# Kernel tuning notes

Measured on AMD Instinct MI355X. Metric: run time of the kernel, lower is better.

## Reference

```python
import jax, jax.numpy as jnp
import numpy as np

N_BCH = 64      # walkers / batch
N_DIM = 64      # total columns in col_var
N_COL = 32      # masked collective variables
N_HIL = 50000   # stored Gaussian hills (history)
WDT = 0.3
HGT0 = 0.02
GAM0 = 10.0
PBC_LEN = 2.0 * np.pi


def gaussian_inner(pbc, prc, cen, hgt, col):
    # col: (B, C); cen, prc: (H, B, C); hgt: (H, B); pbc: (C,)
    diff = col[None, :, :] - cen                      # (H, B, C)
    # minimum-image PBC wrap (only for periodic columns, pbc > 0)
    diff = jnp.where(pbc > 0, diff - pbc * jnp.round(diff / pbc), diff)
    dist2 = jnp.sum(prc * diff * diff, axis=-1)       # (H, B)
    return jnp.sum(hgt * jnp.exp(-0.5 * dist2), axis=0)  # (B,)


def setup_inputs() -> dict:
    key = jax.random.key(0)
    k = jax.random.split(key, 6)
    col_var = jax.random.normal(k[0], (N_BCH, N_DIM), dtype=jnp.float32)
    # hill centers live on the periodic domain
    mtd_cen = jax.random.uniform(k[1], (N_HIL, N_BCH, N_COL), jnp.float32,
                                 -PBC_LEN / 2, PBC_LEN / 2)
    prc_val = 1.0 / (WDT * WDT)
    mtd_prc = jnp.full((N_HIL, N_BCH, N_COL), prc_val, dtype=jnp.float32)
    # well-tempered heights decay over history; random positive heights
    mtd_hgt = HGT0 * jax.random.uniform(k[2], (N_HIL, N_BCH), jnp.float32, 0.1, 1.0)
    kbt = jax.random.uniform(k[3], (N_BCH,), jnp.float32, 0.5, 1.0)
    # module buffers (from __init__ kwargs)
    prc = jnp.full((N_COL,), prc_val, dtype=jnp.float32)   # 1/(wdt*wdt)
    hgt = jnp.asarray(HGT0, dtype=jnp.float32)
    gam = jnp.asarray(GAM0, dtype=jnp.float32)
    pbc = jnp.full((N_COL,), PBC_LEN, dtype=jnp.float32)
    msk = jnp.arange(N_COL, dtype=jnp.int32)
    return {"col_var": col_var, "mtd_cen": mtd_cen, "mtd_prc": mtd_prc,
            "mtd_hgt": mtd_hgt, "kbt": kbt, "prc": prc, "hgt": hgt,
            "gam": gam, "pbc": pbc, "msk": msk}


def reference(col_var, mtd_cen, mtd_prc, mtd_hgt, kbt, prc, hgt, gam, pbc, msk):
    col = col_var[:, msk]                              # (B, C)
    eng = gaussian_inner(pbc, mtd_prc, mtd_cen, mtd_hgt, col)  # (B,)
    # new_gaussian_wtmtd: exponential (well-tempered) height rescale
    det = gam * kbt - kbt                              # (B,)
    hgt_wt = hgt * jnp.exp(-eng / det)                 # (B,)
    prc_new = jnp.broadcast_to(prc[None, :], col.shape)  # (B, C)
    return col, prc_new, hgt_wt
```

## Files before the change

### kernel.cpp

```cpp
#include <hip/hip_runtime.h>

#define N_BCH 64
#define N_DIM 64
#define N_COL 32

typedef float f32x4 __attribute__((ext_vector_type(4)));

__global__ __launch_bounds__(512, 8) void wtmd_main(
    const float* __restrict__ col_var,
    const float* __restrict__ mtd_cen,
    const float* __restrict__ mtd_prc,
    const float* __restrict__ mtd_hgt,
    const float* __restrict__ pbc,
    const int*   __restrict__ msk,
    float*       __restrict__ partial,
    int n_hil)
{
    const int t  = threadIdx.x;
    const int b  = t >> 3;
    const int c0 = (4 * t) & 31;

    float col[4], pb[4], ipb[4];
#pragma unroll
    for (int j = 0; j < 4; ++j) {
        const int c = c0 + j;
        col[j] = col_var[b * N_DIM + msk[c]];
        const float p = pbc[c];
        pb[j]  = p;
        ipb[j] = (p > 0.f) ? (1.0f / p) : 0.f;
    }

    float acc = 0.f;
    const int stride = gridDim.x;

    for (int h = blockIdx.x; h < n_hil; h += stride) {
        const size_t base = (size_t)h * (N_BCH * N_COL) + 4 * (size_t)t;
        const f32x4 cen = __builtin_nontemporal_load((const f32x4*)(mtd_cen + base));
        const f32x4 pr  = __builtin_nontemporal_load((const f32x4*)(mtd_prc + base));
        const float hg  = __builtin_nontemporal_load(mtd_hgt + (size_t)h * N_BCH + b);

        float s = 0.f;
#pragma unroll
        for (int j = 0; j < 4; ++j) {
            float d = col[j] - cen[j];
            d -= pb[j] * rintf(d * ipb[j]);
            s = fmaf(pr[j] * d, d, s);
        }

#pragma unroll
        for (int m = 1; m < 8; m <<= 1)
            s += __shfl_xor(s, m);

        acc += hg * __expf(-0.5f * s);
    }

    if ((t & 7) == 0)
        partial[(size_t)b * stride + blockIdx.x] = acc;
}

__global__ __launch_bounds__(256) void wtmd_epi(
    const float* __restrict__ col_var,
    const float* __restrict__ kbt,
    const float* __restrict__ prc,
    const float* __restrict__ hgt,
    const float* __restrict__ gam,
    const int*   __restrict__ msk,
    const float* __restrict__ partial,
    int nblocks,
    float*       __restrict__ out)
{
    __shared__ float red[256];
    const int t = threadIdx.x;
    const int b = t & 63;
    const int s = t >> 6;

    const float* row = partial + (size_t)b * nblocks;
    float acc = 0.f;
    for (int g = 4 * s; g < nblocks; g += 16) {
        const f32x4 v = *(const f32x4*)(row + g);
        acc += (v[0] + v[1]) + (v[2] + v[3]);
    }
    red[t] = acc;
    __syncthreads();

    if (t < 64) {
        const float eng = (red[t] + red[t + 64]) + (red[t + 128] + red[t + 192]);
        const float k   = kbt[t];
        const float det = gam[0] * k - k;
        out[4096 + t] = hgt[0] * __expf(-eng / det);
    }

    for (int i = t; i < N_BCH * N_COL; i += 256) {
        const int bb = i >> 5;
        const int c  = i & 31;
        out[i]        = col_var[bb * N_DIM + msk[c]];
        out[2048 + i] = prc[c];
    }
}

extern "C" void kernel_launch(void* const* d_in, const int* in_sizes, int n_in,
                              void* d_out, int out_size, void* d_ws, size_t ws_size,
                              hipStream_t stream) {
    const float* col_var = (const float*)d_in[0];
    const float* mtd_cen = (const float*)d_in[1];
    const float* mtd_prc = (const float*)d_in[2];
    const float* mtd_hgt = (const float*)d_in[3];
    const float* kbt     = (const float*)d_in[4];
    const float* prc     = (const float*)d_in[5];
    const float* hgt     = (const float*)d_in[6];
    const float* gam     = (const float*)d_in[7];
    const float* pbc     = (const float*)d_in[8];
    const int*   msk     = (const int*)d_in[9];
    float* out     = (float*)d_out;
    float* partial = (float*)d_ws;

    const int n_hil = in_sizes[3] / N_BCH;

    int nblocks = 1024;
    const size_t per_block = (size_t)N_BCH * sizeof(float);
    if (ws_size < (size_t)nblocks * per_block)
        nblocks = (int)(ws_size / per_block);
    nblocks &= ~3;
    if (nblocks < 4) nblocks = 4;

    wtmd_main<<<nblocks, 512, 0, stream>>>(col_var, mtd_cen, mtd_prc, mtd_hgt,
                                           pbc, msk, partial, n_hil);
    wtmd_epi<<<1, 256, 0, stream>>>(col_var, kbt, prc, hgt, gam, msk,
                                    partial, nblocks, out);
}
```

Measured before the change: 149.8 us.

## Fuse epilogue into main kernel via last-block atomic counter and unroll hill loop by two

Folds the separate reduction/epilogue kernel into the main kernel: each block writes its partials, bumps an atomic counter, and the last block to finish does the final reduction and the exp rescale. The masked column and precision copies move to block 0. The hill loop is also unrolled by two so each thread has two independent load sets in flight. This adds a memset launch for the counter, threadfences and an atomic per block in exchange for dropping the second kernel launch.

```diff
diff --git a/kernel.cpp b/kernel.cpp
--- a/kernel.cpp
+++ b/kernel.cpp
@@ -6,19 +6,35 @@
 
 typedef float f32x4 __attribute__((ext_vector_type(4)));
 
-__global__ __launch_bounds__(512, 8) void wtmd_main(
+__global__ __launch_bounds__(512, 8) void wtmd_fused(
     const float* __restrict__ col_var,
     const float* __restrict__ mtd_cen,
     const float* __restrict__ mtd_prc,
     const float* __restrict__ mtd_hgt,
+    const float* __restrict__ kbt,
+    const float* __restrict__ prc,
+    const float* __restrict__ hgt,
+    const float* __restrict__ gam,
     const float* __restrict__ pbc,
     const int*   __restrict__ msk,
     float*       __restrict__ partial,
-    int n_hil)
+    unsigned*    __restrict__ counter,
+    int n_hil,
+    float*       __restrict__ out)
 {
     const int t  = threadIdx.x;
     const int b  = t >> 3;
     const int c0 = (4 * t) & 31;
+    const int stride = gridDim.x;
+
+    if (blockIdx.x == 0) {
+        for (int i = t; i < N_BCH * N_COL; i += 512) {
+            const int bb = i >> 5;
+            const int c  = i & 31;
+            out[i]        = col_var[bb * N_DIM + msk[c]];
+            out[2048 + i] = prc[c];
+        }
+    }
 
     float col[4], pb[4], ipb[4];
 #pragma unroll
@@ -31,70 +47,85 @@
     }
 
     float acc = 0.f;
-    const int stride = gridDim.x;
+    const int off4t = 4 * t;
 
-    for (int h = blockIdx.x; h < n_hil; h += stride) {
-        const size_t base = (size_t)h * (N_BCH * N_COL) + 4 * (size_t)t;
-        const f32x4 cen = __builtin_nontemporal_load((const f32x4*)(mtd_cen + base));
-        const f32x4 pr  = __builtin_nontemporal_load((const f32x4*)(mtd_prc + base));
-        const float hg  = __builtin_nontemporal_load(mtd_hgt + (size_t)h * N_BCH + b);
+    int h = blockIdx.x;
+    for (; h + stride < n_hil; h += 2 * stride) {
+        const size_t base0 = (size_t)h * (N_BCH * N_COL) + off4t;
+        const size_t base1 = (size_t)(h + stride) * (N_BCH * N_COL) + off4t;
+        const f32x4 cen0 = __builtin_nontemporal_load((const f32x4*)(mtd_cen + base0));
+        const f32x4 pr0  = __builtin_nontemporal_load((const f32x4*)(mtd_prc + base0));
+        const f32x4 cen1 = __builtin_nontemporal_load((const f32x4*)(mtd_cen + base1));
+        const f32x4 pr1  = __builtin_nontemporal_load((const f32x4*)(mtd_prc + base1));
+        const float hg0  = __builtin_nontemporal_load(mtd_hgt + (size_t)h * N_BCH + b);
+        const float hg1  = __builtin_nontemporal_load(mtd_hgt + (size_t)(h + stride) * N_BCH + b);
 
-        float s = 0.f;
+        float s0 = 0.f, s1 = 0.f;
 #pragma unroll
         for (int j = 0; j < 4; ++j) {
-            float d = col[j] - cen[j];
+            float d = col[j] - cen0[j];
             d -= pb[j] * rintf(d * ipb[j]);
-            s = fmaf(pr[j] * d, d, s);
+            s0 = fmaf(pr0[j] * d, d, s0);
+            float e = col[j] - cen1[j];
+            e -= pb[j] * rintf(e * ipb[j]);
+            s1 = fmaf(pr1[j] * e, e, s1);
         }
-
+#pragma unroll
+        for (int m = 1; m < 8; m <<= 1) {
+            s0 += __shfl_xor(s0, m);
+            s1 += __shfl_xor(s1, m);
+        }
+        acc += hg0 * __expf(-0.5f * s0);
+        acc += hg1 * __expf(-0.5f * s1);
+    }
+    if (h < n_hil) {
+        const size_t base0 = (size_t)h * (N_BCH * N_COL) + off4t;
+        const f32x4 cen0 = __builtin_nontemporal_load((const f32x4*)(mtd_cen + base0));
+        const f32x4 pr0  = __builtin_nontemporal_load((const f32x4*)(mtd_prc + base0));
+        const float hg0  = __builtin_nontemporal_load(mtd_hgt + (size_t)h * N_BCH + b);
+        float s0 = 0.f;
+#pragma unroll
+        for (int j = 0; j < 4; ++j) {
+            float d = col[j] - cen0[j];
+            d -= pb[j] * rintf(d * ipb[j]);
+            s0 = fmaf(pr0[j] * d, d, s0);
+        }
 #pragma unroll
         for (int m = 1; m < 8; m <<= 1)
-            s += __shfl_xor(s, m);
-
-        acc += hg * __expf(-0.5f * s);
+            s0 += __shfl_xor(s0, m);
+        acc += hg0 * __expf(-0.5f * s0);
     }
 
     if ((t & 7) == 0)
         partial[(size_t)b * stride + blockIdx.x] = acc;
-}
 
-__global__ __launch_bounds__(256) void wtmd_epi(
-    const float* __restrict__ col_var,
-    const float* __restrict__ kbt,
-    const float* __restrict__ prc,
-    const float* __restrict__ hgt,
-    const float* __restrict__ gam,
-    const int*   __restrict__ msk,
-    const float* __restrict__ partial,
-    int nblocks,
-    float*       __restrict__ out)
-{
-    __shared__ float red[256];
-    const int t = threadIdx.x;
-    const int b = t & 63;
-    const int s = t >> 6;
+    __shared__ unsigned is_last;
+    __threadfence();
+    __syncthreads();
+    if (t == 0)
+        is_last = (atomicAdd(counter, 1u) == (unsigned)(gridDim.x - 1));
+    __syncthreads();
+    if (!is_last) return;
+    __threadfence();
 
-    const float* row = partial + (size_t)b * nblocks;
-    float acc = 0.f;
-    for (int g = 4 * s; g < nblocks; g += 16) {
+    __shared__ float red[512];
+    const int bb = t & 63;
+    const int s  = t >> 6;
+    const float* row = partial + (size_t)bb * stride;
+    float a = 0.f;
+    for (int g = 4 * s; g < stride; g += 32) {
         const f32x4 v = *(const f32x4*)(row + g);
-        acc += (v[0] + v[1]) + (v[2] + v[3]);
+        a += (v[0] + v[1]) + (v[2] + v[3]);
     }
-    red[t] = acc;
+    red[t] = a;
     __syncthreads();
-
     if (t < 64) {
-        const float eng = (red[t] + red[t + 64]) + (red[t + 128] + red[t + 192]);
+        float eng = 0.f;
+#pragma unroll
+        for (int q = 0; q < 8; ++q) eng += red[t + 64 * q];
         const float k   = kbt[t];
         const float det = gam[0] * k - k;
         out[4096 + t] = hgt[0] * __expf(-eng / det);
-    }
-
-    for (int i = t; i < N_BCH * N_COL; i += 256) {
-        const int bb = i >> 5;
-        const int c  = i & 31;
-        out[i]        = col_var[bb * N_DIM + msk[c]];
-        out[2048 + i] = prc[c];
     }
 }
 
@@ -118,13 +149,15 @@
 
     int nblocks = 1024;
     const size_t per_block = (size_t)N_BCH * sizeof(float);
-    if (ws_size < (size_t)nblocks * per_block)
-        nblocks = (int)(ws_size / per_block);
+    if (ws_size < (size_t)nblocks * per_block + sizeof(unsigned))
+        nblocks = (int)((ws_size - sizeof(unsigned)) / per_block);
     nblocks &= ~3;
     if (nblocks < 4) nblocks = 4;
 
-    wtmd_main<<<nblocks, 512, 0, stream>>>(col_var, mtd_cen, mtd_prc, mtd_hgt,
-                                           pbc, msk, partial, n_hil);
-    wtmd_epi<<<1, 256, 0, stream>>>(col_var, kbt, prc, hgt, gam, msk,
-                                    partial, nblocks, out);
+    unsigned* counter = (unsigned*)((char*)d_ws + (size_t)nblocks * per_block);
+    hipMemsetAsync(counter, 0, sizeof(unsigned), stream);
+
+    wtmd_fused<<<nblocks, 512, 0, stream>>>(col_var, mtd_cen, mtd_prc, mtd_hgt,
+                                            kbt, prc, hgt, gam, pbc, msk,
+                                            partial, counter, n_hil, out);
 }
```

Result: slower. 543.9 us (+263.0%).
